# Kernel optimization log

Hardware: AMD Instinct MI355X
Metric: run time of the kernel (lower is better)

Reference implementation:

```python
import jax, jax.numpy as jnp
import numpy as np

B = 65536

def setup_inputs() -> dict:
    key = jax.random.key(0)
    ks = jax.random.split(key, 6)
    x = jax.random.normal(ks[0], (B, 784), dtype=jnp.float32)
    w_conv = jnp.ones((3, 3), dtype=jnp.float32)  # Parameter(ones((3,3)))
    w1 = jax.random.normal(ks[1], (676, 256), dtype=jnp.float32) * 0.04
    b1 = jax.random.normal(ks[2], (256,), dtype=jnp.float32) * 0.01
    w2 = jax.random.normal(ks[3], (256, 10), dtype=jnp.float32) * 0.06
    b2 = jax.random.normal(ks[4], (10,), dtype=jnp.float32) * 0.01
    return {"x": x, "w_conv": w_conv, "w1": w1, "b1": b1, "w2": w2, "b2": b2}

def reference(x, w_conv, w1, b1, w2, b2):
    b = x.shape[0]
    img = x.reshape(b, 1, 28, 28)
    # Convolve() is cross-correlation (no kernel flip), 'VALID': 28->26
    kern = w_conv.reshape(1, 1, 3, 3)
    conv = jax.lax.conv_general_dilated(
        img, kern, window_strides=(1, 1), padding='VALID',
        dimension_numbers=('NCHW', 'OIHW', 'NCHW'))  # (B,1,26,26)
    feat = conv.reshape(b, 676)
    h = jax.nn.relu(feat @ w1 + b1)  # (B,256)
    return h @ w2 + b2               # (B,10)
```

## Files before the change

kernel.cpp:

```cpp
#include <hip/hip_runtime.h>
#include <hip/hip_bf16.h>
#include <stdint.h>

typedef __bf16 bf16;
typedef __attribute__((ext_vector_type(8))) __bf16 bf16x8;
typedef __attribute__((ext_vector_type(4))) float f32x4;

#define KREAL 784
#define NTILES 25
#define TROW   40
#define TILE_ELEMS (256 * TROW)

#define GLOBAL_AS __attribute__((address_space(1)))
#define LDS_AS    __attribute__((address_space(3)))

__global__ __launch_bounds__(256) void prep_w1tt(const float* __restrict__ w_conv,
                                                 const float* __restrict__ w1,
                                                 bf16* __restrict__ W) {
    const int tile = blockIdx.x / TROW;
    const int kk   = blockIdx.x % TROW;
    const int n    = threadIdx.x;
    const int k    = tile * 32 + kk;
    float s = 0.0f;
    if (kk < 32 && k < KREAL) {
        const int r = k / 28, c = k % 28;
        #pragma unroll
        for (int di = 0; di < 3; ++di) {
            const int i = r - di;
            if (i < 0 || i >= 26) continue;
            #pragma unroll
            for (int dj = 0; dj < 3; ++dj) {
                const int j = c - dj;
                if (j < 0 || j >= 26) continue;
                s += w_conv[di * 3 + dj] * w1[(i * 26 + j) * 256 + n];
            }
        }
    }
    W[(size_t)tile * TILE_ELEMS + n * TROW + kk] = (bf16)s;
}

__global__ __launch_bounds__(256, 2) void fused_mlp(
    const float* __restrict__ x,
    const bf16*  __restrict__ W,
    const float* __restrict__ b1,
    const float* __restrict__ w2,
    const float* __restrict__ b2,
    float* __restrict__ out)
{
    __shared__ bf16  Bs[2][TILE_ELEMS];
    __shared__ float w2s[256][10];
    __shared__ float b1s[256];
    __shared__ float b2s[10];

    const int t    = threadIdx.x;
    const int wave = t >> 6;
    const int lane = t & 63;
    const int c    = lane & 15;
    const int q    = lane >> 4;

    const int row0 = blockIdx.x * 128;

    for (int i = t; i < 2560; i += 256) ((float*)w2s)[i] = w2[i];
    b1s[t] = b1[t];
    if (t < 10) b2s[t] = b2[t];

    const float* arow0 = x + (size_t)(row0 + wave * 32 + c) * KREAL + q * 8;
    const float* arow1 = arow0 + (size_t)16 * KREAL;
    const bf16* bsrc = W + (size_t)(wave * 5) * 512 + lane * 8;

    f32x4 acc[2][16];
    #pragma unroll
    for (int mt = 0; mt < 2; ++mt)
        #pragma unroll
        for (int nt = 0; nt < 16; ++nt)
            acc[mt][nt] = (f32x4){0.f, 0.f, 0.f, 0.f};

    #pragma unroll
    for (int j = 0; j < 5; ++j) {
        __builtin_amdgcn_global_load_lds(
            (const GLOBAL_AS void*)(bsrc + j * 512),
            (LDS_AS void*)((char*)&Bs[0][0] + (wave * 5 + j) * 1024), 16, 0, 0);
    }
    float4 f0a = *(const float4*)arow0, f0b = *(const float4*)(arow0 + 4);
    float4 f1a = *(const float4*)arow1, f1b = *(const float4*)(arow1 + 4);
    bf16x8 a0, a1;
    a0[0] = (bf16)f0a.x; a0[1] = (bf16)f0a.y; a0[2] = (bf16)f0a.z; a0[3] = (bf16)f0a.w;
    a0[4] = (bf16)f0b.x; a0[5] = (bf16)f0b.y; a0[6] = (bf16)f0b.z; a0[7] = (bf16)f0b.w;
    a1[0] = (bf16)f1a.x; a1[1] = (bf16)f1a.y; a1[2] = (bf16)f1a.z; a1[3] = (bf16)f1a.w;
    a1[4] = (bf16)f1b.x; a1[5] = (bf16)f1b.y; a1[6] = (bf16)f1b.z; a1[7] = (bf16)f1b.w;
    __syncthreads();

    #pragma unroll 1
    for (int it = 0; it < NTILES; ++it) {
        const int cur = it & 1;
        const bool more = (it + 1) < NTILES;

        if (more) {
            const bf16* bs = bsrc + (size_t)(it + 1) * TILE_ELEMS;
            char* bd = (char*)&Bs[cur ^ 1][0] + wave * 5 * 1024;
            #pragma unroll
            for (int j = 0; j < 5; ++j) {
                __builtin_amdgcn_global_load_lds(
                    (const GLOBAL_AS void*)(bs + j * 512),
                    (LDS_AS void*)(bd + j * 1024), 16, 0, 0);
            }
            const int kn = (it + 1) * 32;
            if (kn + q * 8 < KREAL) {
                const float* p0 = arow0 + kn;
                const float* p1 = arow1 + kn;
                f0a = *(const float4*)p0; f0b = *(const float4*)(p0 + 4);
                f1a = *(const float4*)p1; f1b = *(const float4*)(p1 + 4);
            } else {
                f0a = f0b = f1a = f1b = (float4){0.f, 0.f, 0.f, 0.f};
            }
        }

        #pragma unroll
        for (int nt = 0; nt < 16; ++nt) {
            bf16x8 b = *(const bf16x8*)&Bs[cur][(nt * 16 + c) * TROW + q * 8];
            acc[0][nt] = __builtin_amdgcn_mfma_f32_16x16x32_bf16(a0, b, acc[0][nt], 0, 0, 0);
            acc[1][nt] = __builtin_amdgcn_mfma_f32_16x16x32_bf16(a1, b, acc[1][nt], 0, 0, 0);
        }

        if (more) {
            a0[0] = (bf16)f0a.x; a0[1] = (bf16)f0a.y; a0[2] = (bf16)f0a.z; a0[3] = (bf16)f0a.w;
            a0[4] = (bf16)f0b.x; a0[5] = (bf16)f0b.y; a0[6] = (bf16)f0b.z; a0[7] = (bf16)f0b.w;
            a1[0] = (bf16)f1a.x; a1[1] = (bf16)f1a.y; a1[2] = (bf16)f1a.z; a1[3] = (bf16)f1a.w;
            a1[4] = (bf16)f1b.x; a1[5] = (bf16)f1b.y; a1[6] = (bf16)f1b.z; a1[7] = (bf16)f1b.w;
        }

        __syncthreads();
    }

    float bl[16];
    #pragma unroll
    for (int nt = 0; nt < 16; ++nt) bl[nt] = b1s[nt * 16 + c];

    #pragma unroll
    for (int mt = 0; mt < 2; ++mt)
        #pragma unroll
        for (int nt = 0; nt < 16; ++nt)
            #pragma unroll
            for (int r = 0; r < 4; ++r) {
                float v = acc[mt][nt][r] + bl[nt];
                acc[mt][nt][r] = v > 0.f ? v : 0.f;
            }

    #pragma unroll 1
    for (int j = 0; j < 10; ++j) {
        float wj[16];
        #pragma unroll
        for (int nt = 0; nt < 16; ++nt) wj[nt] = w2s[nt * 16 + c][j];
        const float b2j = b2s[j];
        #pragma unroll
        for (int mt = 0; mt < 2; ++mt)
            #pragma unroll
            for (int r = 0; r < 4; ++r) {
                float s = 0.f;
                #pragma unroll
                for (int nt = 0; nt < 16; ++nt) s += acc[mt][nt][r] * wj[nt];
                s += __shfl_xor(s, 1, 64);
                s += __shfl_xor(s, 2, 64);
                s += __shfl_xor(s, 4, 64);
                s += __shfl_xor(s, 8, 64);
                if (c == j) {
                    const int row = row0 + wave * 32 + mt * 16 + q * 4 + r;
                    out[(size_t)row * 10 + j] = s + b2j;
                }
            }
    }
}

extern "C" void kernel_launch(void* const* d_in, const int* in_sizes, int n_in,
                              void* d_out, int out_size, void* d_ws, size_t ws_size,
                              hipStream_t stream) {
    const float* x  = (const float*)d_in[0];
    const float* wc = (const float*)d_in[1];
    const float* w1 = (const float*)d_in[2];
    const float* b1 = (const float*)d_in[3];
    const float* w2 = (const float*)d_in[4];
    const float* b2 = (const float*)d_in[5];
    float* out = (float*)d_out;
    bf16* W = (bf16*)d_ws;

    prep_w1tt<<<dim3(NTILES * TROW), dim3(256), 0, stream>>>(wc, w1, W);
    fused_mlp<<<dim3(65536 / 128), dim3(256), 0, stream>>>(x, W, b1, w2, b2, out);
}
```

Baseline: 318.4 us.

## Read weight fragments directly from global memory instead of LDS double-buffer

Removes the LDS double-buffered staging of the folded W1 tiles and the per-iteration block barriers. Each lane now loads its bf16x8 B fragment straight from global memory (L2/L1-cached), and the padded tile row shrinks from 40 to 32. This drops the LDS traffic and synchronisation, but MFMA operands now wait on global-load latency with no explicit prefetch, and every wave fetches the full weight tile redundantly through cache.

```diff
diff --git a/kernel.cpp b/kernel.cpp
--- a/kernel.cpp
+++ b/kernel.cpp
@@ -8,21 +8,18 @@
 
 #define KREAL 784
 #define NTILES 25
-#define TROW   40
+#define TROW   32
 #define TILE_ELEMS (256 * TROW)
-
-#define GLOBAL_AS __attribute__((address_space(1)))
-#define LDS_AS    __attribute__((address_space(3)))
 
 __global__ __launch_bounds__(256) void prep_w1tt(const float* __restrict__ w_conv,
                                                  const float* __restrict__ w1,
                                                  bf16* __restrict__ W) {
-    const int tile = blockIdx.x / TROW;
-    const int kk   = blockIdx.x % TROW;
+    const int tile = blockIdx.x >> 5;
+    const int kk   = blockIdx.x & 31;
     const int n    = threadIdx.x;
     const int k    = tile * 32 + kk;
     float s = 0.0f;
-    if (kk < 32 && k < KREAL) {
+    if (k < KREAL) {
         const int r = k / 28, c = k % 28;
         #pragma unroll
         for (int di = 0; di < 3; ++di) {
@@ -47,7 +44,6 @@
     const float* __restrict__ b2,
     float* __restrict__ out)
 {
-    __shared__ bf16  Bs[2][TILE_ELEMS];
     __shared__ float w2s[256][10];
     __shared__ float b1s[256];
     __shared__ float b2s[10];
@@ -66,7 +62,7 @@
 
     const float* arow0 = x + (size_t)(row0 + wave * 32 + c) * KREAL + q * 8;
     const float* arow1 = arow0 + (size_t)16 * KREAL;
-    const bf16* bsrc = W + (size_t)(wave * 5) * 512 + lane * 8;
+    const bf16* wl = W + c * TROW + q * 8;
 
     f32x4 acc[2][16];
     #pragma unroll
@@ -75,12 +71,6 @@
         for (int nt = 0; nt < 16; ++nt)
             acc[mt][nt] = (f32x4){0.f, 0.f, 0.f, 0.f};
 
-    #pragma unroll
-    for (int j = 0; j < 5; ++j) {
-        __builtin_amdgcn_global_load_lds(
-            (const GLOBAL_AS void*)(bsrc + j * 512),
-            (LDS_AS void*)((char*)&Bs[0][0] + (wave * 5 + j) * 1024), 16, 0, 0);
-    }
     float4 f0a = *(const float4*)arow0, f0b = *(const float4*)(arow0 + 4);
     float4 f1a = *(const float4*)arow1, f1b = *(const float4*)(arow1 + 4);
     bf16x8 a0, a1;
@@ -88,22 +78,12 @@
     a0[4] = (bf16)f0b.x; a0[5] = (bf16)f0b.y; a0[6] = (bf16)f0b.z; a0[7] = (bf16)f0b.w;
     a1[0] = (bf16)f1a.x; a1[1] = (bf16)f1a.y; a1[2] = (bf16)f1a.z; a1[3] = (bf16)f1a.w;
     a1[4] = (bf16)f1b.x; a1[5] = (bf16)f1b.y; a1[6] = (bf16)f1b.z; a1[7] = (bf16)f1b.w;
-    __syncthreads();
 
     #pragma unroll 1
     for (int it = 0; it < NTILES; ++it) {
-        const int cur = it & 1;
         const bool more = (it + 1) < NTILES;
 
         if (more) {
-            const bf16* bs = bsrc + (size_t)(it + 1) * TILE_ELEMS;
-            char* bd = (char*)&Bs[cur ^ 1][0] + wave * 5 * 1024;
-            #pragma unroll
-            for (int j = 0; j < 5; ++j) {
-                __builtin_amdgcn_global_load_lds(
-                    (const GLOBAL_AS void*)(bs + j * 512),
-                    (LDS_AS void*)(bd + j * 1024), 16, 0, 0);
-            }
             const int kn = (it + 1) * 32;
             if (kn + q * 8 < KREAL) {
                 const float* p0 = arow0 + kn;
@@ -115,9 +95,10 @@
             }
         }
 
+        const bf16* wt = wl + (size_t)it * TILE_ELEMS;
         #pragma unroll
         for (int nt = 0; nt < 16; ++nt) {
-            bf16x8 b = *(const bf16x8*)&Bs[cur][(nt * 16 + c) * TROW + q * 8];
+            bf16x8 b = *(const bf16x8*)(wt + nt * 16 * TROW);
             acc[0][nt] = __builtin_amdgcn_mfma_f32_16x16x32_bf16(a0, b, acc[0][nt], 0, 0, 0);
             acc[1][nt] = __builtin_amdgcn_mfma_f32_16x16x32_bf16(a1, b, acc[1][nt], 0, 0, 0);
         }
@@ -128,9 +109,9 @@
             a1[0] = (bf16)f1a.x; a1[1] = (bf16)f1a.y; a1[2] = (bf16)f1a.z; a1[3] = (bf16)f1a.w;
             a1[4] = (bf16)f1b.x; a1[5] = (bf16)f1b.y; a1[6] = (bf16)f1b.z; a1[7] = (bf16)f1b.w;
         }
+    }
 
-        __syncthreads();
-    }
+    __syncthreads();
 
     float bl[16];
     #pragma unroll
@@ -183,6 +164,6 @@
     float* out = (float*)d_out;
     bf16* W = (bf16*)d_ws;
 
-    prep_w1tt<<<dim3(NTILES * TROW), dim3(256), 0, stream>>>(wc, w1, W);
+    prep_w1tt<<<dim3(NTILES * 32), dim3(256), 0, stream>>>(wc, w1, W);
     fused_mlp<<<dim3(65536 / 128), dim3(256), 0, stream>>>(x, W, b1, w2, b2, out);
 }
```

Measured after the change: 386.3 us. 21.3% more time.

## Triple-buffer weight tiles with vmcnt-based waits and drop LDS staging of w2/b1

Applied to the files above, without the earlier changes.

Moves the W tile pipeline from double to triple buffering, prefetching two tiles ahead with global_load_lds. It replaces __syncthreads with explicit s_waitcnt vmcnt counts plus raw barriers, so the in-flight loads of the next tile no longer have to drain every iteration. The x loads now run unconditionally with a clamped address and a zeroing multiplier instead of a branch. The w2, b1 and b2 LDS staging is removed and these are read from global memory in the epilogue, which frees LDS for the third buffer. The risk is that the vmcnt count assumes a particular ordering of the x loads and LDS-bound loads, and the epilogue now issues more uncached global reads.

```diff
diff --git a/kernel.cpp b/kernel.cpp
--- a/kernel.cpp
+++ b/kernel.cpp
@@ -47,10 +47,7 @@
     const float* __restrict__ b2,
     float* __restrict__ out)
 {
-    __shared__ bf16  Bs[2][TILE_ELEMS];
-    __shared__ float w2s[256][10];
-    __shared__ float b1s[256];
-    __shared__ float b2s[10];
+    __shared__ bf16 Bs[3][TILE_ELEMS];
 
     const int t    = threadIdx.x;
     const int wave = t >> 6;
@@ -60,10 +57,6 @@
 
     const int row0 = blockIdx.x * 128;
 
-    for (int i = t; i < 2560; i += 256) ((float*)w2s)[i] = w2[i];
-    b1s[t] = b1[t];
-    if (t < 10) b2s[t] = b2[t];
-
     const float* arow0 = x + (size_t)(row0 + wave * 32 + c) * KREAL + q * 8;
     const float* arow1 = arow0 + (size_t)16 * KREAL;
     const bf16* bsrc = W + (size_t)(wave * 5) * 512 + lane * 8;
@@ -75,66 +68,96 @@
         for (int nt = 0; nt < 16; ++nt)
             acc[mt][nt] = (f32x4){0.f, 0.f, 0.f, 0.f};
 
+    float4 f0a = *(const float4*)arow0, f0b = *(const float4*)(arow0 + 4);
+    float4 f1a = *(const float4*)arow1, f1b = *(const float4*)(arow1 + 4);
     #pragma unroll
     for (int j = 0; j < 5; ++j) {
         __builtin_amdgcn_global_load_lds(
             (const GLOBAL_AS void*)(bsrc + j * 512),
             (LDS_AS void*)((char*)&Bs[0][0] + (wave * 5 + j) * 1024), 16, 0, 0);
     }
-    float4 f0a = *(const float4*)arow0, f0b = *(const float4*)(arow0 + 4);
-    float4 f1a = *(const float4*)arow1, f1b = *(const float4*)(arow1 + 4);
+    #pragma unroll
+    for (int j = 0; j < 5; ++j) {
+        __builtin_amdgcn_global_load_lds(
+            (const GLOBAL_AS void*)(bsrc + TILE_ELEMS + j * 512),
+            (LDS_AS void*)((char*)&Bs[1][0] + (wave * 5 + j) * 1024), 16, 0, 0);
+    }
     bf16x8 a0, a1;
     a0[0] = (bf16)f0a.x; a0[1] = (bf16)f0a.y; a0[2] = (bf16)f0a.z; a0[3] = (bf16)f0a.w;
     a0[4] = (bf16)f0b.x; a0[5] = (bf16)f0b.y; a0[6] = (bf16)f0b.z; a0[7] = (bf16)f0b.w;
     a1[0] = (bf16)f1a.x; a1[1] = (bf16)f1a.y; a1[2] = (bf16)f1a.z; a1[3] = (bf16)f1a.w;
     a1[4] = (bf16)f1b.x; a1[5] = (bf16)f1b.y; a1[6] = (bf16)f1b.z; a1[7] = (bf16)f1b.w;
-    __syncthreads();
+
+    asm volatile("s_waitcnt vmcnt(5)" ::: "memory");
+    __builtin_amdgcn_sched_barrier(0);
+    __builtin_amdgcn_s_barrier();
+    __builtin_amdgcn_sched_barrier(0);
 
     #pragma unroll 1
     for (int it = 0; it < NTILES; ++it) {
-        const int cur = it & 1;
-        const bool more = (it + 1) < NTILES;
-
+        const int  cur   = it % 3;
+        const bool more  = (it + 1) < NTILES;
+        const bool more2 = (it + 2) < NTILES;
+
+        float okm = 1.0f;
         if (more) {
-            const bf16* bs = bsrc + (size_t)(it + 1) * TILE_ELEMS;
-            char* bd = (char*)&Bs[cur ^ 1][0] + wave * 5 * 1024;
+            const int kn = (it + 1) * 32;
+            const bool ok = (kn + q * 8) < KREAL;
+            okm = ok ? 1.0f : 0.0f;
+            const int koff = ok ? kn : 0;
+            const float* p0 = arow0 + koff;
+            const float* p1 = arow1 + koff;
+            f0a = *(const float4*)p0; f0b = *(const float4*)(p0 + 4);
+            f1a = *(const float4*)p1; f1b = *(const float4*)(p1 + 4);
+        }
+
+        if (more2) {
+            const bf16* bs = bsrc + (size_t)(it + 2) * TILE_ELEMS;
+            char* bd = (char*)&Bs[(it + 2) % 3][0] + wave * 5 * 1024;
             #pragma unroll
             for (int j = 0; j < 5; ++j) {
                 __builtin_amdgcn_global_load_lds(
                     (const GLOBAL_AS void*)(bs + j * 512),
                     (LDS_AS void*)(bd + j * 1024), 16, 0, 0);
             }
-            const int kn = (it + 1) * 32;
-            if (kn + q * 8 < KREAL) {
-                const float* p0 = arow0 + kn;
-                const float* p1 = arow1 + kn;
-                f0a = *(const float4*)p0; f0b = *(const float4*)(p0 + 4);
-                f1a = *(const float4*)p1; f1b = *(const float4*)(p1 + 4);
+        }
+
+        {
+            const bf16* bb = &Bs[cur][0] + c * TROW + q * 8;
+            #pragma unroll
+            for (int nt = 0; nt < 16; ++nt) {
+                bf16x8 b = *(const bf16x8*)(bb + nt * 16 * TROW);
+                acc[0][nt] = __builtin_amdgcn_mfma_f32_16x16x32_bf16(a0, b, acc[0][nt], 0, 0, 0);
+                acc[1][nt] = __builtin_amdgcn_mfma_f32_16x16x32_bf16(a1, b, acc[1][nt], 0, 0, 0);
+            }
+        }
+
+        if (more) {
+            a0[0] = (bf16)(f0a.x * okm); a0[1] = (bf16)(f0a.y * okm);
+            a0[2] = (bf16)(f0a.z * okm); a0[3] = (bf16)(f0a.w * okm);
+            a0[4] = (bf16)(f0b.x * okm); a0[5] = (bf16)(f0b.y * okm);
+            a0[6] = (bf16)(f0b.z * okm); a0[7] = (bf16)(f0b.w * okm);
+            a1[0] = (bf16)(f1a.x * okm); a1[1] = (bf16)(f1a.y * okm);
+            a1[2] = (bf16)(f1a.z * okm); a1[3] = (bf16)(f1a.w * okm);
+            a1[4] = (bf16)(f1b.x * okm); a1[5] = (bf16)(f1b.y * okm);
+            a1[6] = (bf16)(f1b.z * okm); a1[7] = (bf16)(f1b.w * okm);
+        }
+
+        if (more) {
+            if (more2) {
+                asm volatile("s_waitcnt vmcnt(5)" ::: "memory");
             } else {
-                f0a = f0b = f1a = f1b = (float4){0.f, 0.f, 0.f, 0.f};
-            }
-        }
-
-        #pragma unroll
-        for (int nt = 0; nt < 16; ++nt) {
-            bf16x8 b = *(const bf16x8*)&Bs[cur][(nt * 16 + c) * TROW + q * 8];
-            acc[0][nt] = __builtin_amdgcn_mfma_f32_16x16x32_bf16(a0, b, acc[0][nt], 0, 0, 0);
-            acc[1][nt] = __builtin_amdgcn_mfma_f32_16x16x32_bf16(a1, b, acc[1][nt], 0, 0, 0);
-        }
-
-        if (more) {
-            a0[0] = (bf16)f0a.x; a0[1] = (bf16)f0a.y; a0[2] = (bf16)f0a.z; a0[3] = (bf16)f0a.w;
-            a0[4] = (bf16)f0b.x; a0[5] = (bf16)f0b.y; a0[6] = (bf16)f0b.z; a0[7] = (bf16)f0b.w;
-            a1[0] = (bf16)f1a.x; a1[1] = (bf16)f1a.y; a1[2] = (bf16)f1a.z; a1[3] = (bf16)f1a.w;
-            a1[4] = (bf16)f1b.x; a1[5] = (bf16)f1b.y; a1[6] = (bf16)f1b.z; a1[7] = (bf16)f1b.w;
-        }
-
-        __syncthreads();
+                asm volatile("s_waitcnt vmcnt(0)" ::: "memory");
+            }
+            __builtin_amdgcn_sched_barrier(0);
+            __builtin_amdgcn_s_barrier();
+            __builtin_amdgcn_sched_barrier(0);
+        }
     }
 
     float bl[16];
     #pragma unroll
-    for (int nt = 0; nt < 16; ++nt) bl[nt] = b1s[nt * 16 + c];
+    for (int nt = 0; nt < 16; ++nt) bl[nt] = b1[nt * 16 + c];
 
     #pragma unroll
     for (int mt = 0; mt < 2; ++mt)
@@ -150,8 +173,8 @@
     for (int j = 0; j < 10; ++j) {
         float wj[16];
         #pragma unroll
-        for (int nt = 0; nt < 16; ++nt) wj[nt] = w2s[nt * 16 + c][j];
-        const float b2j = b2s[j];
+        for (int nt = 0; nt < 16; ++nt) wj[nt] = w2[(nt * 16 + c) * 10 + j];
+        const float b2j = b2[j];
         #pragma unroll
         for (int mt = 0; mt < 2; ++mt)
             #pragma unroll
```

Result: no change. 324.6 us (+2.0%).
